# Performance work log

Measured on AMD Instinct MI355X. Metric: run time of the kernel, lower is better.

The kernel has to match this reference:

```python
import jax, jax.numpy as jnp
import numpy as np
from jax import lax

B, R, C = 4, 64, 192          # batch, input_resolution, dim
WN, K = 16, 3                 # ka_win_num, kernel_size
WS = R // 4                   # window_size = R / sqrt(WN) = 16
DN = ('NCHW', 'OIHW', 'NCHW')


def setup_inputs() -> dict:
    key = jax.random.key(0)
    ks = jax.random.split(key, 12)
    rn = lambda k, shp, s=0.05: jax.random.normal(k, shp, dtype=jnp.float32) * s
    return {
        'x': jax.random.normal(ks[0], (B, R * R, C), dtype=jnp.float32),
        'conv1_w': rn(ks[1], (WN * C, 1, K, K), 0.1),
        'dc_w': rn(ks[2], (WN, C)),                             # grouped 1x1 (WN*C -> WN)
        'dc_b': jnp.zeros((WN,), jnp.float32),
        'l1_w': rn(ks[3], (4 * WN, WN)),
        'l1_b': jnp.zeros((4 * WN,), jnp.float32),
        'l2_w': rn(ks[4], (WN, 4 * WN)),
        'l2_b': jnp.zeros((WN,), jnp.float32),
        'gk_w': rn(ks[5], (WN,)),                               # 1x1 conv WN -> 1
        'gk_b': jnp.zeros((1,), jnp.float32),
        'fusion_w': rn(ks[6], (C, (WN + 1) * C)),               # 1x1 conv (WN+1)*C -> C
        'fusion_b': jnp.zeros((C,), jnp.float32),
    }


def _forward(x, conv1_w, dc_w, dc_b, l1_w, l1_b, l2_w, l2_b, gk_w, gk_b,
             fusion_w, fusion_b):
    # pad_feature_map is a no-op since R % WS == 0.
    xw = x.reshape(B, R // WS, WS, R // WS, WS, C)
    xw = xw.transpose(0, 1, 3, 5, 2, 4).reshape(B, WN * C, WS, WS)

    # convlayer1: depthwise conv over all WN*C channels
    y = lax.conv_general_dilated(xw, conv1_w, (1, 1), [(1, 1), (1, 1)],
                                 dimension_numbers=DN,
                                 feature_group_count=WN * C)  # (B, WN*C, WS, WS)

    # WinKernel_Reweight: pool -> grouped 1x1 -> gelu -> 1x1 -> sigmoid
    pooled = y.mean(axis=(2, 3)).reshape(B, WN, C)
    w = jnp.einsum('bwc,wc->bw', pooled, dc_w) + dc_b          # downchannel (groups=WN)
    w = jax.nn.gelu(w @ l1_w.T + l1_b, approximate=False)      # (B, 4*WN)
    w = jax.nn.sigmoid(w @ l2_w.T + l2_b)                      # (B, WN)

    kern = conv1_w.reshape(WN, C, K, K)
    kern = w[:, :, None, None, None] * kern[None]              # (B, WN, C, K, K)

    # global kernel: 1x1 conv across the WN axis
    gk = jnp.einsum('bwcij,w->bcij', kern, gk_w) + gk_b[0]     # (B, C, K, K)
    all_k = jnp.concatenate([kern, gk[:, None]], axis=1)       # (B, WN+1, C, K, K)

    # dynamic depthwise conv on the full map, per sample
    xf = x.reshape(B, R, R, C).transpose(0, 3, 1, 2)           # (B, C, R, R)
    xrep = jnp.tile(xf, (1, WN + 1, 1, 1))                     # (B, (WN+1)*C, R, R)
    kflat = all_k.reshape(B, (WN + 1) * C, 1, K, K)

    def dw(xi, ki):  # xi: ((WN+1)*C, R, R), ki: ((WN+1)*C, 1, K, K)
        return lax.conv_general_dilated(xi[None], ki, (1, 1), [(1, 1), (1, 1)],
                                        dimension_numbers=DN,
                                        feature_group_count=(WN + 1) * C)[0]

    out = jax.vmap(dw)(xrep, kflat)                            # (B, (WN+1)*C, R, R)

    # fusion 1x1 conv -> (B, C, R, R) -> (B, L, C)
    out = jnp.einsum('bdhw,cd->bhwc', out, fusion_w) + fusion_b
    return out.reshape(B, R * R, C)


def reference(x, conv1_w, dc_w, dc_b, l1_w, l1_b, l2_w, l2_b, gk_w, gk_b,
              fusion_w, fusion_b):
    return _forward(x, conv1_w, dc_w, dc_b, l1_w, l1_b, l2_w, l2_b,
                    gk_w, gk_b, fusion_w, fusion_b)
```

## Files before the change

### kernel.cpp

```cpp
#include <hip/hip_runtime.h>
#include <hip/hip_bf16.h>
#include <math.h>

#define B_  4
#define R_  64
#define C_  192
#define WN_ 16


typedef __attribute__((ext_vector_type(8))) short short8;
typedef __attribute__((ext_vector_type(4))) float floatx4;

static __device__ __forceinline__ unsigned short f2bf(float f) {
    union { float f; unsigned u; } v; v.f = f;
    unsigned r = v.u + 0x7fffu + ((v.u >> 16) & 1u);
    return (unsigned short)(r >> 16);
}

static __device__ __forceinline__ void gload_lds16(const void* g, void* l) {
    __builtin_amdgcn_global_load_lds(
        (const __attribute__((address_space(1))) unsigned*)g,
        (__attribute__((address_space(3))) unsigned*)l, 16, 0, 0);
}

__global__ __launch_bounds__(256) void pre_kernel(
        const float* __restrict__ x,
        const float* __restrict__ conv1_w,
        const float* __restrict__ dc_w,
        float* __restrict__ w0p,
        float* __restrict__ cw_t,
        unsigned short* __restrict__ xbf16) {
    __shared__ float part[3];
    int blk = blockIdx.x;
    int tid = threadIdx.x;

    if (blk < 256) {
        int b = blk >> 6, rest = blk & 63, win = rest >> 2, q = rest & 3;
        int wr = win >> 2, wc = win & 3;
        if (tid < 192) {
            const float* xb = x + ((size_t)b * 4096) * C_ + tid;
            float Wsum = 0.f, Rtop = 0.f, Rbot = 0.f, Cleft = 0.f, Cright = 0.f;
            float c00 = 0.f, c0F = 0.f, cF0 = 0.f, cFF = 0.f;
            #pragma unroll
            for (int pr = 0; pr < 4; ++pr) {
                int h = wr * 16 + q * 4 + pr;
                #pragma unroll
                for (int pw = 0; pw < 16; ++pw) {
                    int w = wc * 16 + pw;
                    float v = xb[(size_t)(h * 64 + w) * C_];
                    Wsum += v;
                    if (q == 0 && pr == 0) { Rtop += v; if (pw == 0) c00 = v; if (pw == 15) c0F = v; }
                    if (q == 3 && pr == 3) { Rbot += v; if (pw == 0) cF0 = v; if (pw == 15) cFF = v; }
                    if (pw == 0)  Cleft  += v;
                    if (pw == 15) Cright += v;
                }
            }
            const float* kp = conv1_w + ((size_t)(win * C_ + tid)) * 9;
            float pooled = 0.f;
            #pragma unroll
            for (int i = 0; i < 3; ++i) {
                #pragma unroll
                for (int j = 0; j < 3; ++j) {
                    int di = i - 1, dj = j - 1;
                    float S = Wsum;
                    if (di == -1) S -= Rbot;   else if (di == 1) S -= Rtop;
                    if (dj == -1) S -= Cright; else if (dj == 1) S -= Cleft;
                    if (di == -1 && dj == -1) S += cFF;
                    if (di == -1 && dj ==  1) S += cF0;
                    if (di ==  1 && dj == -1) S += c0F;
                    if (di ==  1 && dj ==  1) S += c00;
                    pooled += kp[i * 3 + j] * S;
                }
            }
            float val = (pooled * (1.f / 256.f)) * dc_w[win * C_ + tid];
            for (int off = 32; off; off >>= 1) val += __shfl_down(val, off, 64);
            if ((tid & 63) == 0) part[tid >> 6] = val;
        }
        __syncthreads();
        if (tid == 0) w0p[blk] = part[0] + part[1] + part[2];
    } else if (blk < 310) {
        int basei = (blk - 256) * 512 + tid * 2;
        #pragma unroll
        for (int e = 0; e < 2; ++e) {
            int o = basei + e;
            int t = o / 3072;
            int r = o - t * 3072;
            cw_t[o] = conv1_w[(size_t)r * 9 + t];
        }
    } else {
        int m = blk - 310;
        int b = m >> 6, hh = m & 63;
        const float* src = x + ((size_t)(b * 4096 + hh * 64)) * C_;
        unsigned short* dst = xbf16 + ((size_t)(b * 64 + hh)) * 12288;
        int px = tid >> 2, c4 = (tid & 3) * 8;
        #pragma unroll
        for (int j = 0; j < 6; ++j) {
            const float* p = src + (size_t)px * C_ + j * 32 + c4;
            float4 v0 = *(const float4*)p;
            float4 v1 = *(const float4*)(p + 4);
            short8 o;
            o[0] = (short)f2bf(v0.x); o[1] = (short)f2bf(v0.y);
            o[2] = (short)f2bf(v0.z); o[3] = (short)f2bf(v0.w);
            o[4] = (short)f2bf(v1.x); o[5] = (short)f2bf(v1.y);
            o[6] = (short)f2bf(v1.z); o[7] = (short)f2bf(v1.w);
            *(short8*)(dst + j * 2048 + px * 32 + c4) = o;
        }
    }
}

__global__ __launch_bounds__(192) void weff_kernel(
        const float* __restrict__ cw_t,
        const float* __restrict__ gk_w,
        const float* __restrict__ gk_b,
        const float* __restrict__ fusion_w,
        const float* __restrict__ w0p,
        const float* __restrict__ dc_b,
        const float* __restrict__ l1_w,
        const float* __restrict__ l1_b,
        const float* __restrict__ l2_w,
        const float* __restrict__ l2_b,
        unsigned short* __restrict__ Wl) {
    __shared__ float hbuf[64];
    __shared__ float s_sh[16];
    int blk = blockIdx.x;
    int b = blk / C_, co = blk % C_;
    int tid = threadIdx.x;

    if (tid < 64) {
        float a = l1_b[tid];
        #pragma unroll
        for (int w = 0; w < 16; ++w) {
            float w0 = w0p[b * 64 + w * 4 + 0] + w0p[b * 64 + w * 4 + 1]
                     + w0p[b * 64 + w * 4 + 2] + w0p[b * 64 + w * 4 + 3];
            a += (w0 + dc_b[w]) * l1_w[tid * 16 + w];
        }
        hbuf[tid] = 0.5f * a * (1.f + erff(a * 0.70710678118654752f));
    }
    __syncthreads();
    if (tid < 16) {
        float a2 = l2_b[tid];
        #pragma unroll
        for (int k = 0; k < 64; ++k) a2 += hbuf[k] * l2_w[tid * 64 + k];
        s_sh[tid] = 1.f / (1.f + expf(-a2));
    }
    __syncthreads();

    int ci = tid;
    float fg = fusion_w[(size_t)co * 3264 + 16 * C_ + ci];
    float acc[9];
    float g0 = fg * gk_b[0];
    #pragma unroll
    for (int t = 0; t < 9; ++t) acc[t] = g0;
    for (int w = 0; w < 16; ++w) {
        float coef = (fusion_w[(size_t)co * 3264 + w * C_ + ci] + fg * gk_w[w]) * s_sh[w];
        #pragma unroll
        for (int t = 0; t < 9; ++t)
            acc[t] += coef * cw_t[t * 3072 + w * C_ + ci];
    }
    #pragma unroll
    for (int t = 0; t < 9; ++t) {
        int kc = ci >> 5, cio = ci & 31;
        Wl[((((size_t)(b * 9 + t)) * 6 + kc) * C_ + co) * 32 + cio] = f2bf(acc[t]);
    }
}

__global__ __launch_bounds__(256, 1) void conv_kernel(
        const unsigned short* __restrict__ xbf16,
        const unsigned short* __restrict__ Wl,
        const float* __restrict__ fusion_b,
        float* __restrict__ out) {
    __shared__ unsigned short Asm[2 * 3 * 3 * 66 * 32];
    const int n = blockIdx.x;
    const int g = (n & 7) * 32 + (n >> 3);
    const int b = g >> 6, h = g & 63;
    const int tid = threadIdx.x;
    const int wv = tid >> 6, lane = tid & 63;
    const int lo = lane & 15, quad = lane >> 4;
    const int n0 = wv * 48;

    const short* wp = (const short*)Wl;
    int Bbase[3];
    #pragma unroll
    for (int nt = 0; nt < 3; ++nt)
        Bbase[nt] = (b * 54 * C_ + n0 + nt * 16 + lo) * 32 + quad * 8;
    int Alds[4];
    #pragma unroll
    for (int mt = 0; mt < 4; ++mt)
        Alds[mt] = (mt * 16 + lo + 1) * 32 + quad * 8;

    floatx4 acc[4][3];
    #pragma unroll
    for (int mt = 0; mt < 4; ++mt)
        #pragma unroll
        for (int nt = 0; nt < 3; ++nt)
            acc[mt][nt] = (floatx4){0.f, 0.f, 0.f, 0.f};

    const short8 z8 = {0, 0, 0, 0, 0, 0, 0, 0};
    if (h == 0 || h == 63) {
        for (int c = tid; c < 4752; c += 256)
            *(short8*)(Asm + c * 8) = z8;
    } else if (tid < 144) {
        int buf = tid / 72, u = tid % 72;
        int loc = u >> 2, j = u & 3;
        int r = loc / 6, rem = loc % 6, kcl = rem >> 1, px = (rem & 1) * 65;
        *(short8*)(Asm + buf * 19008 + ((r * 3 + kcl) * 66 + px) * 32 + j * 8) = z8;
    }
    __syncthreads();

    auto issue_phase = [&](int buf, int ph) {
        const int kc0 = ph * 3;
        #pragma unroll
        for (int i = 0; i < 9; ++i) {
            int c = wv * 9 + i;
            int r = c / 12, kcl = (c % 12) >> 2, q = c & 3;
            int hr = h - 1 + r;
            if (hr >= 0 && hr < 64) {
                const unsigned short* src = xbf16
                    + ((((size_t)(b * 64 + hr)) * 6 + (kc0 + kcl)) << 11)
                    + (q << 9) + lane * 8;
                unsigned short* dst = Asm + buf * 19008
                    + ((r * 3 + kcl) * 66 + 1) * 32 + q * 512;
                gload_lds16(src, dst);
            }
        }
    };

    short8 Bb[5][3], Ab[3][4];
    auto loadB = [&](int t, int slot) {
        int ph = t / 27, tt = t - ph * 27;
        int tap = tt / 3, kcl = tt - tap * 3;
        int s = tap * 6 + ph * 3 + kcl;
        #pragma unroll
        for (int nt = 0; nt < 3; ++nt)
            Bb[slot][nt] = *(const short8*)(wp + Bbase[nt] + s * (C_ * 32));
    };
    auto loadA = [&](int t, int slot) {
        int ph = t / 27, tt = t - ph * 27;
        int tap = tt / 3, kcl = tt - tap * 3;
        int dh = tap / 3, dw = tap % 3 - 1;
        const short* As = (const short*)Asm + ph * 19008;
        int base = ((dh * 3 + kcl) * 66 + dw) * 32;
        #pragma unroll
        for (int mt = 0; mt < 4; ++mt)
            Ab[slot][mt] = *(const short8*)(As + base + Alds[mt]);
    };

    issue_phase(0, 0);
    loadB(0, 0); loadB(1, 1); loadB(2, 2); loadB(3, 3);
    __syncthreads();
    issue_phase(1, 1);
    loadA(0, 0); loadA(1, 1);

    #pragma unroll
    for (int t = 0; t < 27; ++t) {
        loadB(t + 4, (t + 4) % 5);
        if (t + 2 < 27) loadA(t + 2, (t + 2) % 3);
        #pragma unroll
        for (int mt = 0; mt < 4; ++mt)
            #pragma unroll
            for (int nt = 0; nt < 3; ++nt)
                acc[mt][nt] = __builtin_amdgcn_mfma_f32_16x16x32_bf16(
                    Ab[t % 3][mt], Bb[t % 5][nt], acc[mt][nt], 0, 0, 0);
    }

    __syncthreads();
    loadA(27, 0); loadA(28, 1);

    #pragma unroll
    for (int t = 27; t < 54; ++t) {
        if (t + 4 < 54) loadB(t + 4, (t + 4) % 5);
        if (t + 2 < 54) loadA(t + 2, (t + 2) % 3);
        #pragma unroll
        for (int mt = 0; mt < 4; ++mt)
            #pragma unroll
            for (int nt = 0; nt < 3; ++nt)
                acc[mt][nt] = __builtin_amdgcn_mfma_f32_16x16x32_bf16(
                    Ab[t % 3][mt], Bb[t % 5][nt], acc[mt][nt], 0, 0, 0);
    }

    #pragma unroll
    for (int nt = 0; nt < 3; ++nt) {
        const int co = n0 + nt * 16 + lo;
        const float fb = fusion_b[co];
        #pragma unroll
        for (int mt = 0; mt < 4; ++mt) {
            #pragma unroll
            for (int r = 0; r < 4; ++r) {
                const int px = mt * 16 + quad * 4 + r;
                out[((size_t)(b * 4096 + h * 64 + px)) * C_ + co] = acc[mt][nt][r] + fb;
            }
        }
    }
}

extern "C" void kernel_launch(void* const* d_in, const int* in_sizes, int n_in,
                              void* d_out, int out_size, void* d_ws, size_t ws_size,
                              hipStream_t stream) {
    const float* x        = (const float*)d_in[0];
    const float* conv1_w  = (const float*)d_in[1];
    const float* dc_w     = (const float*)d_in[2];
    const float* dc_b     = (const float*)d_in[3];
    const float* l1_w     = (const float*)d_in[4];
    const float* l1_b     = (const float*)d_in[5];
    const float* l2_w     = (const float*)d_in[6];
    const float* l2_b     = (const float*)d_in[7];
    const float* gk_w     = (const float*)d_in[8];
    const float* gk_b     = (const float*)d_in[9];
    const float* fusion_w = (const float*)d_in[10];
    const float* fusion_b = (const float*)d_in[11];
    float* out = (float*)d_out;

    char* ws = (char*)d_ws;
    float* w0p  = (float*)ws;
    float* cw_t = (float*)(ws + 1024);
    unsigned short* Wl = (unsigned short*)(ws + 1024 + 110592);
    unsigned short* xbf16 = (unsigned short*)(ws + 1024 + 110592 + 2654208);

    hipLaunchKernelGGL(pre_kernel, dim3(566), dim3(256), 0, stream,
                       x, conv1_w, dc_w, w0p, cw_t, xbf16);
    hipLaunchKernelGGL(weff_kernel, dim3(B_ * C_), dim3(192), 0, stream,
                       cw_t, gk_w, gk_b, fusion_w, w0p, dc_b, l1_w, l1_b, l2_w, l2_b, Wl);
    hipLaunchKernelGGL(conv_kernel, dim3(256), dim3(256), 0, stream,
                       xbf16, Wl, fusion_b, out);
}
```

Measured before the change: 118.3 us.

## Retile conv kernel so each block computes two output rows for half the channels

The conv block tile changes from one image row with all 192 output channels to two rows with 96 output channels. The 4 waves are arranged as 2 rows by 2 channel groups, and the shared input halo (4 rows) is staged in dynamic LDS of about 99KB. The aim is to reuse the staged input rows across two output rows, which cuts redundant halo loads from 3 rows per output row to 2. The cost is that each block reads only half the weights, larger LDS needs a dynamic shared memory attribute, and weight loads are duplicated across the row pairs.

```diff
diff --git a/kernel.cpp b/kernel.cpp
--- a/kernel.cpp
+++ b/kernel.cpp
@@ -169,20 +169,22 @@
         const unsigned short* __restrict__ Wl,
         const float* __restrict__ fusion_b,
         float* __restrict__ out) {
-    __shared__ unsigned short Asm[2 * 3 * 3 * 66 * 32];
+    extern __shared__ unsigned short Asm[];
     const int n = blockIdx.x;
     const int g = (n & 7) * 32 + (n >> 3);
-    const int b = g >> 6, h = g & 63;
+    const int b = g >> 6, ch = (g >> 5) & 1, rp = g & 31;
+    const int r0 = rp * 2;
     const int tid = threadIdx.x;
     const int wv = tid >> 6, lane = tid & 63;
     const int lo = lane & 15, quad = lane >> 4;
-    const int n0 = wv * 48;
+    const int wr = wv >> 1;
+    const int c0 = ch * 96 + (wv & 1) * 48;
 
     const short* wp = (const short*)Wl;
     int Bbase[3];
     #pragma unroll
     for (int nt = 0; nt < 3; ++nt)
-        Bbase[nt] = (b * 54 * C_ + n0 + nt * 16 + lo) * 32 + quad * 8;
+        Bbase[nt] = (b * 54 * C_ + c0 + nt * 16 + lo) * 32 + quad * 8;
     int Alds[4];
     #pragma unroll
     for (int mt = 0; mt < 4; ++mt)
@@ -196,30 +198,38 @@
             acc[mt][nt] = (floatx4){0.f, 0.f, 0.f, 0.f};
 
     const short8 z8 = {0, 0, 0, 0, 0, 0, 0, 0};
-    if (h == 0 || h == 63) {
-        for (int c = tid; c < 4752; c += 256)
-            *(short8*)(Asm + c * 8) = z8;
-    } else if (tid < 144) {
-        int buf = tid / 72, u = tid % 72;
+    if (rp == 0) {
+        for (int c = tid; c < 1584; c += 256) {
+            int b2 = c / 792, rem = c % 792, kcl = rem / 264, j = rem % 264;
+            *(short8*)(Asm + b2 * 25344 + kcl * 2112 + j * 8) = z8;
+        }
+    }
+    if (rp == 31) {
+        for (int c = tid; c < 1584; c += 256) {
+            int b2 = c / 792, rem = c % 792, kcl = rem / 264, j = rem % 264;
+            *(short8*)(Asm + b2 * 25344 + (9 + kcl) * 2112 + j * 8) = z8;
+        }
+    }
+    if (tid < 192) {
+        int b2 = tid / 96, u = tid % 96;
         int loc = u >> 2, j = u & 3;
-        int r = loc / 6, rem = loc % 6, kcl = rem >> 1, px = (rem & 1) * 65;
-        *(short8*)(Asm + buf * 19008 + ((r * 3 + kcl) * 66 + px) * 32 + j * 8) = z8;
+        int lr = loc / 6, rem = loc % 6, kcl = rem >> 1, px = (rem & 1) * 65;
+        *(short8*)(Asm + b2 * 25344 + ((lr * 3 + kcl) * 66 + px) * 32 + j * 8) = z8;
     }
     __syncthreads();
 
     auto issue_phase = [&](int buf, int ph) {
         const int kc0 = ph * 3;
-        #pragma unroll
-        for (int i = 0; i < 9; ++i) {
-            int c = wv * 9 + i;
-            int r = c / 12, kcl = (c % 12) >> 2, q = c & 3;
-            int hr = h - 1 + r;
-            if (hr >= 0 && hr < 64) {
+        const int hr = r0 - 1 + wv;
+        if (hr >= 0 && hr < 64) {
+            #pragma unroll
+            for (int i = 0; i < 12; ++i) {
+                int kcl = i >> 2, q = i & 3;
                 const unsigned short* src = xbf16
                     + ((((size_t)(b * 64 + hr)) * 6 + (kc0 + kcl)) << 11)
                     + (q << 9) + lane * 8;
-                unsigned short* dst = Asm + buf * 19008
-                    + ((r * 3 + kcl) * 66 + 1) * 32 + q * 512;
+                unsigned short* dst = Asm + buf * 25344
+                    + ((wv * 3 + kcl) * 66 + 1) * 32 + q * 512;
                 gload_lds16(src, dst);
             }
         }
@@ -238,8 +248,8 @@
         int ph = t / 27, tt = t - ph * 27;
         int tap = tt / 3, kcl = tt - tap * 3;
         int dh = tap / 3, dw = tap % 3 - 1;
-        const short* As = (const short*)Asm + ph * 19008;
-        int base = ((dh * 3 + kcl) * 66 + dw) * 32;
+        const short* As = (const short*)Asm + ph * 25344;
+        int base = (((wr + dh) * 3 + kcl) * 66 + dw) * 32;
         #pragma unroll
         for (int mt = 0; mt < 4; ++mt)
             Ab[slot][mt] = *(const short8*)(As + base + Alds[mt]);
@@ -278,16 +288,17 @@
                     Ab[t % 3][mt], Bb[t % 5][nt], acc[mt][nt], 0, 0, 0);
     }
 
+    const int row = r0 + wr;
     #pragma unroll
     for (int nt = 0; nt < 3; ++nt) {
-        const int co = n0 + nt * 16 + lo;
+        const int co = c0 + nt * 16 + lo;
         const float fb = fusion_b[co];
         #pragma unroll
         for (int mt = 0; mt < 4; ++mt) {
             #pragma unroll
             for (int r = 0; r < 4; ++r) {
                 const int px = mt * 16 + quad * 4 + r;
-                out[((size_t)(b * 4096 + h * 64 + px)) * C_ + co] = acc[mt][nt][r] + fb;
+                out[((size_t)(b * 4096 + row * 64 + px)) * C_ + co] = acc[mt][nt][r] + fb;
             }
         }
     }
@@ -316,10 +327,17 @@
     unsigned short* Wl = (unsigned short*)(ws + 1024 + 110592);
     unsigned short* xbf16 = (unsigned short*)(ws + 1024 + 110592 + 2654208);
 
+    static bool attr_done = false;
+    if (!attr_done) {
+        hipFuncSetAttribute(reinterpret_cast<const void*>(conv_kernel),
+                            hipFuncAttributeMaxDynamicSharedMemorySize, 101376);
+        attr_done = true;
+    }
+
     hipLaunchKernelGGL(pre_kernel, dim3(566), dim3(256), 0, stream,
                        x, conv1_w, dc_w, w0p, cw_t, xbf16);
     hipLaunchKernelGGL(weff_kernel, dim3(B_ * C_), dim3(192), 0, stream,
                        cw_t, gk_w, gk_b, fusion_w, w0p, dc_b, l1_w, l1_b, l2_w, l2_b, Wl);
-    hipLaunchKernelGGL(conv_kernel, dim3(256), dim3(256), 0, stream,
+    hipLaunchKernelGGL(conv_kernel, dim3(256), dim3(256), 101376, stream,
                        xbf16, Wl, fusion_b, out);
 }
```

Result: no change. 120.7 us (+2.0%).
